# Kernel optimization log

Measured on AMD Instinct MI355X. Metric: run time of the kernel, lower is better.

The kernel has to match this reference:

```python
import jax, jax.numpy as jnp
import numpy as np

EMBED_DIM = 768
NUM_HEADS = 12
HEAD_DIM = EMBED_DIM // NUM_HEADS
SCALE = HEAD_DIM ** -0.5


def setup_inputs() -> dict:
    key = jax.random.key(0)
    k_x, k_qkv, k_proj, k_pb = jax.random.split(key, 4)
    x = jax.random.normal(k_x, (2, 4096, EMBED_DIM), dtype=jnp.float32)
    # nn.Linear weights stored as [out, in]; qkv_bias=False -> no qkv bias
    W_qkv = jax.random.normal(k_qkv, (3 * EMBED_DIM, EMBED_DIM), dtype=jnp.float32) * (EMBED_DIM ** -0.5)
    W_proj = jax.random.normal(k_proj, (EMBED_DIM, EMBED_DIM), dtype=jnp.float32) * (EMBED_DIM ** -0.5)
    b_proj = jax.random.normal(k_pb, (EMBED_DIM,), dtype=jnp.float32) * 0.01
    return {"x": x, "W_qkv": W_qkv, "W_proj": W_proj, "b_proj": b_proj}


def reference(x, W_qkv, W_proj, b_proj):
    bs, seq_len, _ = x.shape
    qkv = jnp.einsum("bse,fe->bsf", x, W_qkv)  # [B,S,3E]
    q, k, v = jnp.split(qkv, 3, axis=-1)
    # [B,S,E] -> [B,H,S,D]
    def to_heads(t):
        return t.reshape(bs, seq_len, NUM_HEADS, HEAD_DIM).transpose(0, 2, 1, 3)
    q, k, v = to_heads(q), to_heads(k), to_heads(v)
    scores = jnp.einsum("bhqd,bhkd->bhqk", q, k) * SCALE
    attn = jax.nn.softmax(scores, axis=-1)  # dropout p=0.0 -> identity
    out = jnp.einsum("bhqk,bhkd->bhqd", attn, v)
    out = out.transpose(0, 2, 1, 3).reshape(bs, seq_len, EMBED_DIM)
    return jnp.einsum("bse,fe->bsf", out, W_proj) + b_proj
```

## Files before the change

### kernel.cpp

```cpp
#include <hip/hip_runtime.h>
#include <stdint.h>


typedef unsigned short u16;
typedef __attribute__((ext_vector_type(8))) short short8;
typedef __attribute__((ext_vector_type(4))) float float4v;

#define C2F 0.18033688011112042f

#if __has_builtin(__builtin_amdgcn_exp2f)
#define QSCALE C2F
#define FEXP(x) __builtin_amdgcn_exp2f(x)
#else
#define QSCALE 0.125f
#define FEXP(x) __expf(x)
#endif

__device__ __forceinline__ u16 f2bf(float f) {
  uint32_t u = __float_as_uint(f);
  u += 0x7FFFu + ((u >> 16) & 1u);
  return (u16)(u >> 16);
}
__device__ __forceinline__ float4v mfma16(short8 a, short8 b, float4v c) {
  return __builtin_amdgcn_mfma_f32_16x16x32_bf16(a, b, c, 0, 0, 0);
}
__device__ __forceinline__ short8 ld8(const u16* p) { return *(const short8*)p; }
__device__ __forceinline__ void st8(u16* p, short8 v) { *(short8*)p = v; }

__device__ __forceinline__ void dma16(const u16* g, u16* l) {
  __builtin_amdgcn_global_load_lds(
      (const __attribute__((address_space(1))) void*)g,
      (__attribute__((address_space(3))) void*)l, 16, 0, 0);
}

__device__ __forceinline__ uint32_t pk2(float lo, float hi) {
  return __builtin_amdgcn_perm(__float_as_uint(hi) + 0x8000u,
                               __float_as_uint(lo) + 0x8000u, 0x07060302u);
}
__device__ __forceinline__ short8 pack8(float4 a, float4 b) {
  union { short8 s; uint32_t u[4]; } r;
  r.u[0] = pk2(a.x, a.y); r.u[1] = pk2(a.z, a.w);
  r.u[2] = pk2(b.x, b.y); r.u[3] = pk2(b.z, b.w);
  return r.s;
}

__global__ __launch_bounds__(256, 3) void k_gemm_qkv(
    const float* __restrict__ x, const float* __restrict__ Wq,
    u16* __restrict__ qkv2, u16* __restrict__ Vt) {
  __shared__ u16 sA[128 * 64];
  __shared__ u16 sB[128 * 64];
  const int m0 = blockIdx.x * 128;
  const int f0 = blockIdx.y * 128;
  const bool vmode = (f0 >= 1536);
  const int tid = threadIdx.x;
  const int w = tid >> 6, lane = tid & 63;
  const int quad = lane >> 4, r = lane & 15;
  const int srow = lane >> 3, sc = lane & 7;

  float4v acc[4][4];
#pragma unroll
  for (int i = 0; i < 4; ++i)
#pragma unroll
    for (int j = 0; j < 4; ++j) acc[i][j] = (float4v){0.f, 0.f, 0.f, 0.f};

  float4 px[4][2], pw[4][2];
#pragma unroll
  for (int t = 0; t < 4; ++t) {
    const int row = 32 * w + 8 * t + srow;
    const float4* xa = (const float4*)x + (size_t)(m0 + row) * 192 + 2 * sc;
    const float4* wa = (const float4*)Wq + (size_t)(f0 + row) * 192 + 2 * sc;
    px[t][0] = xa[0]; px[t][1] = xa[1];
    pw[t][0] = wa[0]; pw[t][1] = wa[1];
  }

  for (int kt = 0; kt < 12; ++kt) {
#pragma unroll
    for (int t = 0; t < 4; ++t) {
      const int row = 32 * w + 8 * t + srow;
      st8(sA + row * 64 + 8 * (sc ^ srow), pack8(px[t][0], px[t][1]));
      st8(sB + row * 64 + 8 * (sc ^ srow), pack8(pw[t][0], pw[t][1]));
    }
    __syncthreads();
    if (kt + 1 < 12) {
#pragma unroll
      for (int t = 0; t < 4; ++t) {
        const int row = 32 * w + 8 * t + srow;
        const float4* xa = (const float4*)x + (size_t)(m0 + row) * 192 + (kt + 1) * 16 + 2 * sc;
        const float4* wa = (const float4*)Wq + (size_t)(f0 + row) * 192 + (kt + 1) * 16 + 2 * sc;
        px[t][0] = xa[0]; px[t][1] = xa[1];
        pw[t][0] = wa[0]; pw[t][1] = wa[1];
      }
    }
    const u16* At = vmode ? sB : sA;
    const u16* Bt = vmode ? sA : sB;
#pragma unroll
    for (int ks = 0; ks < 2; ++ks) {
      short8 a[4], b[4];
#pragma unroll
      for (int i = 0; i < 4; ++i) {
        const int ra = 64 * (w >> 1) + 16 * i + r;
        const int rb = 64 * (w & 1) + 16 * i + r;
        a[i] = ld8(At + ra * 64 + 8 * ((4 * ks + quad) ^ (ra & 7)));
        b[i] = ld8(Bt + rb * 64 + 8 * ((4 * ks + quad) ^ (rb & 7)));
      }
#pragma unroll
      for (int mi = 0; mi < 4; ++mi)
#pragma unroll
        for (int nf = 0; nf < 4; ++nf) acc[mi][nf] = mfma16(a[mi], b[nf], acc[mi][nf]);
    }
    __syncthreads();
  }

  if (!vmode) {
    const float qs = (f0 < 768) ? QSCALE : 1.0f;
#pragma unroll
    for (int mi = 0; mi < 4; ++mi) {
      const int m = m0 + 64 * (w >> 1) + 16 * mi + 4 * quad;
#pragma unroll
      for (int nf = 0; nf < 4; ++nf) {
        const int f = f0 + 64 * (w & 1) + 16 * nf + r;
#pragma unroll
        for (int reg = 0; reg < 4; ++reg)
          qkv2[(size_t)(m + reg) * 1536 + f] = f2bf(acc[mi][nf][reg] * qs);
      }
    }
  } else {
#pragma unroll
    for (int mi = 0; mi < 4; ++mi) {
      const int vcol = f0 - 1536 + 64 * (w >> 1) + 16 * mi + 4 * quad;
#pragma unroll
      for (int nf = 0; nf < 4; ++nf) {
        const int m = m0 + 64 * (w & 1) + 16 * nf + r;
        const int mp = (m & ~0x1C) | ((m & 0x0C) << 1) | ((m & 0x10) >> 2);
#pragma unroll
        for (int reg = 0; reg < 4; ++reg)
          Vt[(size_t)(vcol + reg) * 8192 + mp] = f2bf(acc[mi][nf][reg]);
      }
    }
  }
}

__global__ __launch_bounds__(256, 4) void k_flash(
    const u16* __restrict__ qkv2, const u16* __restrict__ Vt, u16* __restrict__ attn) {
  __shared__ u16 sK[2][64 * 64];
  __shared__ u16 sV[2][64 * 64];
  const int id = blockIdx.x;
  const int xcd = id & 7, slot = id >> 3;
  const int bh = xcd * 3 + (slot >> 5);
  const int qt = slot & 31;
  const int b = bh / 12, h = bh % 12;
  const int tid = threadIdx.x;
  const int w = tid >> 6, lane = tid & 63;
  const int quad = lane >> 4, r = lane & 15;
  const int srow = lane >> 3, sc = lane & 7;
  const u16* Qg = qkv2 + (size_t)b * 4096 * 1536 + h * 64;
  const u16* Kg = Qg + 768;
  const u16* Vg = Vt + (size_t)h * 64 * 8192 + (size_t)b * 4096;

  u16* sQ = &sK[0][0];
#pragma unroll
  for (int t = 0; t < 4; ++t) {
    const int row = 32 * t + (tid >> 3);
    st8(sQ + row * 64 + 8 * (sc ^ (row & 7)),
        ld8(Qg + (size_t)(qt * 128 + row) * 1536 + 8 * sc));
  }
  __syncthreads();
  short8 qf[2][2];
#pragma unroll
  for (int sub = 0; sub < 2; ++sub)
#pragma unroll
    for (int ks = 0; ks < 2; ++ks) {
      const int row = 32 * w + 16 * sub + r;
      qf[sub][ks] = ld8(sQ + row * 64 + 8 * ((4 * ks + quad) ^ (r & 7)));
    }
  __syncthreads();

  const int gsw = 8 * (sc ^ srow);
  const u16* kgp = Kg + (size_t)(8 * w + srow) * 1536 + gsw;
  const u16* vgp = Vg + (size_t)(8 * w + srow) * 8192 + gsw;
  const int ldso = w * 512;

  const int kfo0 = 64 * r + 8 * ((quad) ^ (r & 7));
  const int kfo1 = 64 * r + 8 * ((4 + quad) ^ (r & 7));
  const int pvoJ0 = 64 * r + 8 * ((0 + quad) ^ (r & 7));
  const int pvoJ1 = 64 * r + 8 * ((4 + quad) ^ (r & 7));

  const short8 ones8 = {0x3F80, 0x3F80, 0x3F80, 0x3F80,
                        0x3F80, 0x3F80, 0x3F80, 0x3F80};
  const float4v ZERO4 = {0.f, 0.f, 0.f, 0.f};
  float4v acc_l[2];
  float4v acc_o[2][4];
#pragma unroll
  for (int sub = 0; sub < 2; ++sub) {
    acc_l[sub] = ZERO4;
#pragma unroll
    for (int nf = 0; nf < 4; ++nf) acc_o[sub][nf] = ZERO4;
  }

  dma16(kgp, &sK[0][ldso]);
  dma16(kgp + (size_t)32 * 1536, &sK[0][2048 + ldso]);
  dma16(vgp, &sV[0][ldso]);
  dma16(vgp + (size_t)32 * 8192, &sV[0][2048 + ldso]);
  kgp += (size_t)64 * 1536;
  vgp += 64;

  int buf = 0;
  for (int kt = 0; kt < 64; ++kt) {
    __syncthreads();
    if (kt + 1 < 64) {
      const int nb = buf ^ 1;
      dma16(kgp, &sK[nb][ldso]);
      dma16(kgp + (size_t)32 * 1536, &sK[nb][2048 + ldso]);
      dma16(vgp, &sV[nb][ldso]);
      dma16(vgp + (size_t)32 * 8192, &sV[nb][2048 + ldso]);
      kgp += (size_t)64 * 1536;
      vgp += 64;
    }
    const u16* kb0 = &sK[buf][0] + kfo0;
    const u16* kb1 = &sK[buf][0] + kfo1;
    const u16* vb0 = &sV[buf][0];

    float4v s0[4], s1[4];
#pragma unroll
    for (int n4 = 0; n4 < 4; ++n4) {
      short8 kf = ld8(kb0 + 1024 * n4);
      s0[n4] = mfma16(kf, qf[0][0], ZERO4);
      s1[n4] = mfma16(kf, qf[1][0], ZERO4);
    }
#pragma unroll
    for (int n4 = 0; n4 < 4; ++n4) {
      short8 kf = ld8(kb1 + 1024 * n4);
      s0[n4] = mfma16(kf, qf[0][1], s0[n4]);
      s1[n4] = mfma16(kf, qf[1][1], s1[n4]);
    }

#pragma unroll
    for (int J = 0; J < 2; ++J) {
      union { short8 s8; uint32_t u[4]; } a0, a1;
#pragma unroll
      for (int h4 = 0; h4 < 2; ++h4) {
        const int n4 = 2 * J + h4;
#pragma unroll
        for (int reg = 0; reg < 4; ++reg) {
          s0[n4][reg] = FEXP(s0[n4][reg]);
          s1[n4][reg] = FEXP(s1[n4][reg]);
        }
        a0.u[2 * h4 + 0] = pk2(s0[n4][0], s0[n4][1]);
        a0.u[2 * h4 + 1] = pk2(s0[n4][2], s0[n4][3]);
        a1.u[2 * h4 + 0] = pk2(s1[n4][0], s1[n4][1]);
        a1.u[2 * h4 + 1] = pk2(s1[n4][2], s1[n4][3]);
      }

      const u16* vbn = vb0 + (J ? pvoJ1 : pvoJ0);
#pragma unroll
      for (int nf = 0; nf < 4; ++nf) {
        short8 bv = ld8(vbn + 1024 * nf);
        acc_o[0][nf] = mfma16(a0.s8, bv, acc_o[0][nf]);
        acc_o[1][nf] = mfma16(a1.s8, bv, acc_o[1][nf]);
      }
      acc_l[0] = mfma16(a0.s8, ones8, acc_l[0]);
      acc_l[1] = mfma16(a1.s8, ones8, acc_l[1]);
    }
    buf ^= 1;
  }

#pragma unroll
  for (int sub = 0; sub < 2; ++sub)
#pragma unroll
    for (int reg = 0; reg < 4; ++reg) {
      const float iv = 1.0f / acc_l[sub][reg];
      const int q = qt * 128 + 32 * w + 16 * sub + 4 * quad + reg;
#pragma unroll
      for (int nf = 0; nf < 4; ++nf)
        attn[(size_t)(b * 4096 + q) * 768 + h * 64 + 16 * nf + r] =
            f2bf(acc_o[sub][nf][reg] * iv);
    }
}

__global__ __launch_bounds__(256, 3) void k_gemm_out(
    const u16* __restrict__ attn, const float* __restrict__ Wp,
    const float* __restrict__ bp, float* __restrict__ out) {
  __shared__ u16 sA[128 * 64];
  __shared__ u16 sB[128 * 64];
  const int m0 = blockIdx.x * 128;
  const int f0 = blockIdx.y * 128;
  const int tid = threadIdx.x;
  const int w = tid >> 6, lane = tid & 63;
  const int quad = lane >> 4, r = lane & 15;
  const int srow = lane >> 3, sc = lane & 7;

  float4v acc[4][4];
#pragma unroll
  for (int i = 0; i < 4; ++i)
#pragma unroll
    for (int j = 0; j < 4; ++j) acc[i][j] = (float4v){0.f, 0.f, 0.f, 0.f};

  short8 pa[4];
  float4 pw[4][2];
#pragma unroll
  for (int t = 0; t < 4; ++t) {
    const int row = 32 * w + 8 * t + srow;
    pa[t] = ld8(attn + (size_t)(m0 + row) * 768 + 8 * sc);
    const float4* wa = (const float4*)Wp + (size_t)(f0 + row) * 192 + 2 * sc;
    pw[t][0] = wa[0]; pw[t][1] = wa[1];
  }

  for (int kt = 0; kt < 12; ++kt) {
#pragma unroll
    for (int t = 0; t < 4; ++t) {
      const int row = 32 * w + 8 * t + srow;
      st8(sA + row * 64 + 8 * (sc ^ srow), pa[t]);
      st8(sB + row * 64 + 8 * (sc ^ srow), pack8(pw[t][0], pw[t][1]));
    }
    __syncthreads();
    if (kt + 1 < 12) {
#pragma unroll
      for (int t = 0; t < 4; ++t) {
        const int row = 32 * w + 8 * t + srow;
        pa[t] = ld8(attn + (size_t)(m0 + row) * 768 + (kt + 1) * 64 + 8 * sc);
        const float4* wa = (const float4*)Wp + (size_t)(f0 + row) * 192 + (kt + 1) * 16 + 2 * sc;
        pw[t][0] = wa[0]; pw[t][1] = wa[1];
      }
    }
#pragma unroll
    for (int ks = 0; ks < 2; ++ks) {
      short8 a[4], b[4];
#pragma unroll
      for (int i = 0; i < 4; ++i) {
        const int ra = 64 * (w >> 1) + 16 * i + r;
        const int rb = 64 * (w & 1) + 16 * i + r;
        a[i] = ld8(sA + ra * 64 + 8 * ((4 * ks + quad) ^ (ra & 7)));
        b[i] = ld8(sB + rb * 64 + 8 * ((4 * ks + quad) ^ (rb & 7)));
      }
#pragma unroll
      for (int mi = 0; mi < 4; ++mi)
#pragma unroll
        for (int nf = 0; nf < 4; ++nf) acc[mi][nf] = mfma16(a[mi], b[nf], acc[mi][nf]);
    }
    __syncthreads();
  }

#pragma unroll
  for (int mi = 0; mi < 4; ++mi) {
    const int m = m0 + 64 * (w >> 1) + 16 * mi + 4 * quad;
#pragma unroll
    for (int nf = 0; nf < 4; ++nf) {
      const int f = f0 + 64 * (w & 1) + 16 * nf + r;
      const float bias = bp[f];
#pragma unroll
      for (int reg = 0; reg < 4; ++reg)
        out[(size_t)(m + reg) * 768 + f] = acc[mi][nf][reg] + bias;
    }
  }
}

__global__ void k_copy(const uint4* __restrict__ src, uint4* __restrict__ dst, int n16) {
  int i = blockIdx.x * blockDim.x + threadIdx.x;
  if (i < n16) dst[i] = src[i];
}

extern "C" void kernel_launch(void* const* d_in, const int* in_sizes, int n_in,
                              void* d_out, int out_size, void* d_ws, size_t ws_size,
                              hipStream_t stream) {
  const float* x  = (const float*)d_in[0];
  const float* Wq = (const float*)d_in[1];
  const float* Wp = (const float*)d_in[2];
  const float* bp = (const float*)d_in[3];

  u16* qkv2 = (u16*)d_ws;
  u16* Vt   = qkv2 + (size_t)8192 * 1536;

  const bool big_ws = ws_size >= (size_t)48 * 1024 * 1024;
  u16* attn  = big_ws ? Vt + (size_t)768 * 8192 : (u16*)d_out;
  float* ogem = big_ws ? (float*)d_out : (float*)qkv2;

  hipLaunchKernelGGL(k_gemm_qkv, dim3(64, 18), dim3(256), 0, stream, x, Wq, qkv2, Vt);
  hipLaunchKernelGGL(k_flash, dim3(768), dim3(256), 0, stream, qkv2, Vt, attn);
  hipLaunchKernelGGL(k_gemm_out, dim3(64, 6), dim3(256), 0, stream, attn, Wp, bp, ogem);
  if (!big_ws) {
    const int n16 = (8192 * 768 * 4) / 16;
    hipLaunchKernelGGL(k_copy, dim3(n16 / 256), dim3(256), 0, stream,
                       (const uint4*)ogem, (uint4*)d_out, n16);
  }
}
```

Before: 266.8 us.

## Split flash attention work across 8 waves with 16 query rows each

The flash-attention kernel now launches 512 threads (8 waves) per block instead of 4, and each wave handles 16 query rows instead of 32. The K/V tile loads are spread across the extra waves, so each thread issues half as many DMA copies. Per-wave registers and MFMA chains shrink, which raises the number of resident waves and helps hide latency. In exchange, each K/V fragment read from LDS now feeds only one MFMA instead of two, doubling LDS read traffic per FLOP, and block-wide barriers now synchronise more waves.

```diff
diff --git a/kernel.cpp b/kernel.cpp
--- a/kernel.cpp
+++ b/kernel.cpp
@@ -140,7 +140,7 @@
   }
 }
 
-__global__ __launch_bounds__(256, 4) void k_flash(
+__global__ __launch_bounds__(512, 6) void k_flash(
     const u16* __restrict__ qkv2, const u16* __restrict__ Vt, u16* __restrict__ attn) {
   __shared__ u16 sK[2][64 * 64];
   __shared__ u16 sV[2][64 * 64];
@@ -159,20 +159,18 @@
 
   u16* sQ = &sK[0][0];
 #pragma unroll
-  for (int t = 0; t < 4; ++t) {
-    const int row = 32 * t + (tid >> 3);
+  for (int t = 0; t < 2; ++t) {
+    const int row = 64 * t + (tid >> 3);
     st8(sQ + row * 64 + 8 * (sc ^ (row & 7)),
         ld8(Qg + (size_t)(qt * 128 + row) * 1536 + 8 * sc));
   }
   __syncthreads();
-  short8 qf[2][2];
-#pragma unroll
-  for (int sub = 0; sub < 2; ++sub)
-#pragma unroll
-    for (int ks = 0; ks < 2; ++ks) {
-      const int row = 32 * w + 16 * sub + r;
-      qf[sub][ks] = ld8(sQ + row * 64 + 8 * ((4 * ks + quad) ^ (r & 7)));
-    }
+  short8 qf[2];
+#pragma unroll
+  for (int ks = 0; ks < 2; ++ks) {
+    const int row = 16 * w + r;
+    qf[ks] = ld8(sQ + row * 64 + 8 * ((4 * ks + quad) ^ (r & 7)));
+  }
   __syncthreads();
 
   const int gsw = 8 * (sc ^ srow);
@@ -188,19 +186,13 @@
   const short8 ones8 = {0x3F80, 0x3F80, 0x3F80, 0x3F80,
                         0x3F80, 0x3F80, 0x3F80, 0x3F80};
   const float4v ZERO4 = {0.f, 0.f, 0.f, 0.f};
-  float4v acc_l[2];
-  float4v acc_o[2][4];
-#pragma unroll
-  for (int sub = 0; sub < 2; ++sub) {
-    acc_l[sub] = ZERO4;
-#pragma unroll
-    for (int nf = 0; nf < 4; ++nf) acc_o[sub][nf] = ZERO4;
-  }
+  float4v acc_l = ZERO4;
+  float4v acc_o[4];
+#pragma unroll
+  for (int nf = 0; nf < 4; ++nf) acc_o[nf] = ZERO4;
 
   dma16(kgp, &sK[0][ldso]);
-  dma16(kgp + (size_t)32 * 1536, &sK[0][2048 + ldso]);
   dma16(vgp, &sV[0][ldso]);
-  dma16(vgp + (size_t)32 * 8192, &sV[0][2048 + ldso]);
   kgp += (size_t)64 * 1536;
   vgp += 64;
 
@@ -210,9 +202,7 @@
     if (kt + 1 < 64) {
       const int nb = buf ^ 1;
       dma16(kgp, &sK[nb][ldso]);
-      dma16(kgp + (size_t)32 * 1536, &sK[nb][2048 + ldso]);
       dma16(vgp, &sV[nb][ldso]);
-      dma16(vgp + (size_t)32 * 8192, &sV[nb][2048 + ldso]);
       kgp += (size_t)64 * 1536;
       vgp += 64;
     }
@@ -220,61 +210,50 @@
     const u16* kb1 = &sK[buf][0] + kfo1;
     const u16* vb0 = &sV[buf][0];
 
-    float4v s0[4], s1[4];
+    float4v s[4];
 #pragma unroll
     for (int n4 = 0; n4 < 4; ++n4) {
       short8 kf = ld8(kb0 + 1024 * n4);
-      s0[n4] = mfma16(kf, qf[0][0], ZERO4);
-      s1[n4] = mfma16(kf, qf[1][0], ZERO4);
+      s[n4] = mfma16(kf, qf[0], ZERO4);
     }
 #pragma unroll
     for (int n4 = 0; n4 < 4; ++n4) {
       short8 kf = ld8(kb1 + 1024 * n4);
-      s0[n4] = mfma16(kf, qf[0][1], s0[n4]);
-      s1[n4] = mfma16(kf, qf[1][1], s1[n4]);
+      s[n4] = mfma16(kf, qf[1], s[n4]);
     }
 
 #pragma unroll
     for (int J = 0; J < 2; ++J) {
-      union { short8 s8; uint32_t u[4]; } a0, a1;
+      union { short8 s8; uint32_t u[4]; } a;
 #pragma unroll
       for (int h4 = 0; h4 < 2; ++h4) {
         const int n4 = 2 * J + h4;
 #pragma unroll
-        for (int reg = 0; reg < 4; ++reg) {
-          s0[n4][reg] = FEXP(s0[n4][reg]);
-          s1[n4][reg] = FEXP(s1[n4][reg]);
-        }
-        a0.u[2 * h4 + 0] = pk2(s0[n4][0], s0[n4][1]);
-        a0.u[2 * h4 + 1] = pk2(s0[n4][2], s0[n4][3]);
-        a1.u[2 * h4 + 0] = pk2(s1[n4][0], s1[n4][1]);
-        a1.u[2 * h4 + 1] = pk2(s1[n4][2], s1[n4][3]);
+        for (int reg = 0; reg < 4; ++reg) s[n4][reg] = FEXP(s[n4][reg]);
+        a.u[2 * h4 + 0] = pk2(s[n4][0], s[n4][1]);
+        a.u[2 * h4 + 1] = pk2(s[n4][2], s[n4][3]);
       }
 
       const u16* vbn = vb0 + (J ? pvoJ1 : pvoJ0);
 #pragma unroll
       for (int nf = 0; nf < 4; ++nf) {
         short8 bv = ld8(vbn + 1024 * nf);
-        acc_o[0][nf] = mfma16(a0.s8, bv, acc_o[0][nf]);
-        acc_o[1][nf] = mfma16(a1.s8, bv, acc_o[1][nf]);
-      }
-      acc_l[0] = mfma16(a0.s8, ones8, acc_l[0]);
-      acc_l[1] = mfma16(a1.s8, ones8, acc_l[1]);
+        acc_o[nf] = mfma16(a.s8, bv, acc_o[nf]);
+      }
+      acc_l = mfma16(a.s8, ones8, acc_l);
     }
     buf ^= 1;
   }
 
 #pragma unroll
-  for (int sub = 0; sub < 2; ++sub)
-#pragma unroll
-    for (int reg = 0; reg < 4; ++reg) {
-      const float iv = 1.0f / acc_l[sub][reg];
-      const int q = qt * 128 + 32 * w + 16 * sub + 4 * quad + reg;
-#pragma unroll
-      for (int nf = 0; nf < 4; ++nf)
-        attn[(size_t)(b * 4096 + q) * 768 + h * 64 + 16 * nf + r] =
-            f2bf(acc_o[sub][nf][reg] * iv);
-    }
+  for (int reg = 0; reg < 4; ++reg) {
+    const float iv = 1.0f / acc_l[reg];
+    const int q = qt * 128 + 16 * w + 4 * quad + reg;
+#pragma unroll
+    for (int nf = 0; nf < 4; ++nf)
+      attn[(size_t)(b * 4096 + q) * 768 + h * 64 + 16 * nf + r] =
+          f2bf(acc_o[nf][reg] * iv);
+  }
 }
 
 __global__ __launch_bounds__(256, 3) void k_gemm_out(
@@ -375,7 +354,7 @@
   float* ogem = big_ws ? (float*)d_out : (float*)qkv2;
 
   hipLaunchKernelGGL(k_gemm_qkv, dim3(64, 18), dim3(256), 0, stream, x, Wq, qkv2, Vt);
-  hipLaunchKernelGGL(k_flash, dim3(768), dim3(256), 0, stream, qkv2, Vt, attn);
+  hipLaunchKernelGGL(k_flash, dim3(768), dim3(512), 0, stream, qkv2, Vt, attn);
   hipLaunchKernelGGL(k_gemm_out, dim3(64, 6), dim3(256), 0, stream, attn, Wp, bp, ogem);
   if (!big_ws) {
     const int n16 = (8192 * 768 * 4) / 16;
```

Result: no change. 268.9 us (+0.8%).
